# Kernel optimization log

Measured on AMD Instinct MI355X. Metric: run time of the kernel, lower is better.

The kernel has to match this reference:

```python
import jax, jax.numpy as jnp
import numpy as np

K = 4096       # num_codebook_vectors
D = 256        # latent_dim
BETA = 0.25


def setup_inputs() -> dict:
    key = jax.random.key(0)
    k1, k2 = jax.random.split(key)
    z = jax.random.normal(k1, (16, D, 64, 64), dtype=jnp.float32)
    # nn.Embedding init: uniform(-1/K, 1/K)
    emb = jax.random.uniform(k2, (K, D), dtype=jnp.float32, minval=-1.0 / K, maxval=1.0 / K)
    return {"z": z, "emb": emb}


def reference(z, emb):
    B, C, H, W = z.shape
    zp = jnp.transpose(z, (0, 2, 3, 1))            # [B,H,W,C]
    zf = zp.reshape(-1, C)                          # [N,C]
    # squared L2 distances: ||z||^2 + ||e||^2 - 2 z.e
    d = (jnp.sum(zf * zf, axis=1, keepdims=True)
         + jnp.sum(emb * emb, axis=1)
         - 2.0 * jnp.matmul(zf, emb.T))             # [N,K]
    idx = jnp.argmin(d, axis=1)                     # [N]
    z_q = jnp.take(emb, idx, axis=0).reshape(zp.shape)  # [B,H,W,C]
    loss = (jnp.mean((jax.lax.stop_gradient(z_q) - zp) ** 2)
            + BETA * jnp.mean((z_q - jax.lax.stop_gradient(zp)) ** 2))
    # straight-through estimator
    z_q = zp + jax.lax.stop_gradient(z_q - zp)
    z_q = jnp.transpose(z_q, (0, 3, 1, 2))          # back to NCHW
    return z_q, idx, loss
```

## Files before the change

kernel.cpp:

```cpp
#include <hip/hip_runtime.h>
#include <math.h>

#define KCODES 4096
#define DIM    256
#define HW     4096
#define NPIX   65536
#define NQ     16777216
#define EPSW   3.0e-4f

typedef _Float16 f16x8 __attribute__((ext_vector_type(8)));
typedef float    f32x4 __attribute__((ext_vector_type(4)));

#define SWZ(x) ((x) ^ ((((x) >> 6) & 7) << 4))

static __device__ __forceinline__ void gld16(const void* g, void* l) {
    __builtin_amdgcn_global_load_lds(
        (const __attribute__((address_space(1))) void*)g,
        (__attribute__((address_space(3))) void*)l, 16, 0, 0);
}

#define INS4(V, I, dd, kk) do { \
  if ((dd) < V[3]) { \
    if ((dd) < V[1]) { \
      V[3]=V[2]; I[3]=I[2]; V[2]=V[1]; I[2]=I[1]; \
      if ((dd) < V[0]) { V[1]=V[0]; I[1]=I[0]; V[0]=(dd); I[0]=(kk); } \
      else             { V[1]=(dd); I[1]=(kk); } \
    } else { \
      if ((dd) < V[2]) { V[3]=V[2]; I[3]=I[2]; V[2]=(dd); I[2]=(kk); } \
      else             { V[3]=(dd); I[3]=(kk); } \
    } } } while(0)

#define INS8(V, I, dd, kk) do { \
  if ((dd) < V[7]) { \
    if ((dd) < V[3]) { \
      V[7]=V[6];I[7]=I[6];V[6]=V[5];I[6]=I[5];V[5]=V[4];I[5]=I[4];V[4]=V[3];I[4]=I[3]; \
      if ((dd) < V[1]) { \
        V[3]=V[2];I[3]=I[2];V[2]=V[1];I[2]=I[1]; \
        if ((dd) < V[0]) { V[1]=V[0];I[1]=I[0];V[0]=(dd);I[0]=(kk); } \
        else             { V[1]=(dd);I[1]=(kk); } \
      } else { \
        if ((dd) < V[2]) { V[3]=V[2];I[3]=I[2];V[2]=(dd);I[2]=(kk); } \
        else             { V[3]=(dd);I[3]=(kk); } \
      } \
    } else { \
      if ((dd) < V[5]) { \
        V[7]=V[6];I[7]=I[6];V[6]=V[5];I[6]=I[5]; \
        if ((dd) < V[4]) { V[5]=V[4];I[5]=I[4];V[4]=(dd);I[4]=(kk); } \
        else             { V[5]=(dd);I[5]=(kk); } \
      } else { \
        if ((dd) < V[6]) { V[7]=V[6];I[7]=I[6];V[6]=(dd);I[6]=(kk); } \
        else             { V[7]=(dd);I[7]=(kk); } \
      } \
    } } } while(0)

__global__ __launch_bounds__(256) void ee_np_kernel(const float* __restrict__ emb,
                                                    float* __restrict__ ee) {
#pragma clang fp contract(off)
    const int k = blockIdx.x * 256 + threadIdx.x;
    const float* a = emb + (size_t)k * DIM;
    float res[2];
    #pragma unroll
    for (int h = 0; h < 2; ++h) {
        const float* b = a + h * 128;
        float r[8];
        #pragma unroll
        for (int j = 0; j < 8; ++j) { const float x = b[j]; r[j] = x * x; }
        for (int i = 8; i < 128; i += 8) {
            #pragma unroll
            for (int j = 0; j < 8; ++j) { const float x = b[i + j]; r[j] += x * x; }
        }
        res[h] = ((r[0] + r[1]) + (r[2] + r[3])) + ((r[4] + r[5]) + (r[6] + r[7]));
    }
    ee[k] = res[0] + res[1];
}

__global__ __launch_bounds__(256) void zz_np_kernel(const float* __restrict__ z,
                                                    float* __restrict__ zz) {
#pragma clang fp contract(off)
    const int n  = blockIdx.x * 256 + threadIdx.x;
    const int b  = n >> 12;
    const int hw = n & (HW - 1);
    const float* base = z + (size_t)b * DIM * HW + hw;
    float res[2];
    #pragma unroll
    for (int h = 0; h < 2; ++h) {
        const float* p = base + (size_t)(h * 128) * HW;
        float r[8];
        #pragma unroll
        for (int j = 0; j < 8; ++j) { const float x = p[(size_t)j * HW]; r[j] = x * x; }
        for (int i = 8; i < 128; i += 8) {
            #pragma unroll
            for (int j = 0; j < 8; ++j) { const float x = p[(size_t)(i + j) * HW]; r[j] += x * x; }
        }
        res[h] = ((r[0] + r[1]) + (r[2] + r[3])) + ((r[4] + r[5]) + (r[6] + r[7]));
    }
    zz[n] = res[0] + res[1];
}

__device__ float np_dist(const float* __restrict__ z, const float* __restrict__ emb,
                         const float* __restrict__ zz, const float* __restrict__ ee,
                         int n, int k) {
    const int b = n >> 12, hw = n & (HW - 1);
    const float* zp = z + (size_t)b * DIM * HW + hw;
    const float* ep = emb + (size_t)k * DIM;
    float m = 0.0f;
    for (int i = 0; i < DIM; ++i) m = fmaf(zp[(size_t)i * HW], ep[i], m);
    const float t = zz[n] + ee[k];
    return t - 2.0f * m;
}

__global__ __launch_bounds__(256) void cvt_emb_kernel(const float* __restrict__ emb,
                                                      ushort* __restrict__ eh) {
    const int t = threadIdx.x;
    const int k = blockIdx.x * 4 + (t >> 6);
    const int seg = t & 63;
    const float4 v = *reinterpret_cast<const float4*>(emb + (size_t)k * DIM + seg * 4);
    union H4 { _Float16 h[4]; short4 s; } uh;
    const float vv[4] = {v.x, v.y, v.z, v.w};
    #pragma unroll
    for (int j = 0; j < 4; ++j) uh.h[j] = (_Float16)(vv[j] * 4096.0f);
    const int s = seg >> 3;
    const int y  = (k & 127) * 64 + (seg & 7) * 8;
    const int ys = y ^ ((k & 7) << 4);
    const size_t addr = (size_t)(k >> 7) * 32768 + s * 4096 + (ys >> 1);
    *reinterpret_cast<short4*>(eh + addr) = uh.s;
}

__global__ __launch_bounds__(256) void cvt_z_kernel(const float* __restrict__ z,
                                                    ushort* __restrict__ zh) {
    __shared__ float ls[64][65];
    const int t = threadIdx.x;
    const int bid = blockIdx.x;
    const int b = bid >> 8, cc = (bid >> 6) & 3, hh = bid & 63;
    const int col = t & 63, r0 = t >> 6;
    #pragma unroll
    for (int i = 0; i < 16; ++i) {
        const int r = i * 4 + r0;
        ls[r][col] = z[((size_t)(b * DIM + cc * 64 + r)) * HW + hh * 64 + col];
    }
    __syncthreads();
    const int pxl = t >> 2, cseg = t & 3;
    const int px = b * HW + hh * 64 + pxl;
    const int sg = cc * 2 + (cseg >> 1);
    union H8 { _Float16 h[8]; int4 v; } ha, hb;
    #pragma unroll
    for (int j = 0; j < 16; ++j) {
        const float val = ls[cseg * 16 + j][pxl];
        if (j < 8) ha.h[j] = (_Float16)val;
        else       hb.h[j - 8] = (_Float16)val;
    }
    const size_t chunk = (size_t)(px >> 7) * 32768 + sg * 4096;
    const int y1  = (px & 127) * 64 + (cseg & 1) * 32;
    const int msk = (px & 7) << 4;
    *reinterpret_cast<int4*>(zh + chunk + ((y1 ^ msk) >> 1))        = ha.v;
    *reinterpret_cast<int4*>(zh + chunk + (((y1 + 16) ^ msk) >> 1)) = hb.v;
}

__global__ __launch_bounds__(256, 2) void gemm_kernel(const ushort* __restrict__ eh,
                                                      const ushort* __restrict__ zh,
                                                      const float* __restrict__ ee,
                                                      const float* __restrict__ zz,
                                                      float* __restrict__ top8v,
                                                      int* __restrict__ top8i,
                                                      float* __restrict__ m3f) {
    __shared__ __align__(16) char zt[65536];
    __shared__ __align__(16) char et[2][8192];

    const int t = threadIdx.x;
    const int lane = t & 63, w = t >> 6, wr = w >> 1, wc = w & 1;
    const int l15 = lane & 15, l4 = lane >> 4;
    const int px0 = blockIdx.x * 128;
    const int lo = t * 16;
    const int wb = w * 1024;

    {
        const char* zg = (const char*)zh + (size_t)blockIdx.x * 65536;
        #pragma unroll
        for (int i = 0; i < 16; ++i)
            gld16(zg + i * 4096 + lo, zt + i * 4096 + wb);
        const char* eg = (const char*)eh;
        gld16(eg + lo,        et[0] + wb);
        gld16(eg + 4096 + lo, et[0] + 4096 + wb);
    }
    float zzr[4];
    #pragma unroll
    for (int ni = 0; ni < 4; ++ni) zzr[ni] = zz[px0 + wc * 64 + ni * 16 + l15];
    __syncthreads();

    float Tv[4][4]; int Ti[4][4];
    #pragma unroll
    for (int ni = 0; ni < 4; ++ni)
        #pragma unroll
        for (int j = 0; j < 4; ++j) { Tv[ni][j] = 3.0e38f; Ti[ni][j] = 0; }

    f32x4 acc[4][4];
    float eer[4][4];
    int cur = 0;

    for (int t7 = 0; t7 < 256; ++t7) {
        const int p = t7 >> 3, s = t7 & 7;
        if (t7 < 255) {
            const char* eg = (const char*)eh + (size_t)(t7 + 1) * 8192;
            gld16(eg + lo,        et[cur ^ 1] + wb);
            gld16(eg + 4096 + lo, et[cur ^ 1] + 4096 + wb);
        }
        if (s == 0) {
            #pragma unroll
            for (int mi = 0; mi < 4; ++mi) {
                #pragma unroll
                for (int r = 0; r < 4; ++r)
                    eer[mi][r] = ee[p * 128 + wr * 64 + mi * 16 + l4 * 4 + r];
                #pragma unroll
                for (int ni = 0; ni < 4; ++ni)
                    acc[mi][ni] = (f32x4){0.0f, 0.0f, 0.0f, 0.0f};
            }
        }
        f16x8 bH[4];
        #pragma unroll
        for (int ni = 0; ni < 4; ++ni) {
            const int ob = s * 8192 + SWZ((wc * 64 + ni * 16 + l15) * 64 + l4 * 16);
            bH[ni] = *reinterpret_cast<const f16x8*>(zt + ob);
        }
        #pragma unroll
        for (int mi = 0; mi < 4; ++mi) {
            const int oa = SWZ((wr * 64 + mi * 16 + l15) * 64 + l4 * 16);
            const f16x8 aH = *reinterpret_cast<const f16x8*>(et[cur] + oa);
            #pragma unroll
            for (int ni = 0; ni < 4; ++ni)
                acc[mi][ni] = __builtin_amdgcn_mfma_f32_16x16x32_f16(aH, bH[ni], acc[mi][ni], 0, 0, 0);
        }
        if (s == 7) {
            #pragma unroll
            for (int ni = 0; ni < 4; ++ni) {
                const float zzc = zzr[ni];
                #pragma unroll
                for (int mi = 0; mi < 4; ++mi) {
                    #pragma unroll
                    for (int r = 0; r < 4; ++r) {
                        const float tt = zzc + eer[mi][r];
                        const float d = fmaf(acc[mi][ni][r], -4.8828125e-4f, tt);
                        const int k = p * 128 + wr * 64 + mi * 16 + l4 * 4 + r;
                        INS4(Tv[ni], Ti[ni], d, k);
                    }
                }
            }
        }
        __syncthreads();
        cur ^= 1;
    }

    float (*mv)[128][8]  = reinterpret_cast<float (*)[128][8]>(&zt[0]);
    int   (*mi_)[128][8] = reinterpret_cast<int (*)[128][8]>(&zt[16384]);
    float (*m3s)[128]    = reinterpret_cast<float (*)[128]>(&zt[32768]);

    #pragma unroll
    for (int ni = 0; ni < 4; ++ni) {
        float fv[8]; int fi[8];
        #pragma unroll
        for (int j = 0; j < 4; ++j) { fv[j] = Tv[ni][j]; fi[j] = Ti[ni][j]; }
        #pragma unroll
        for (int j = 4; j < 8; ++j) { fv[j] = 3.0e38f; fi[j] = 0; }
        float m3 = Tv[ni][3];
        #pragma unroll
        for (int m = 16; m <= 32; m <<= 1) {
            float ov[8]; int oi[8];
            #pragma unroll
            for (int j = 0; j < 8; ++j) {
                ov[j] = __shfl_xor(fv[j], m, 64);
                oi[j] = __shfl_xor(fi[j], m, 64);
            }
            const float om = __shfl_xor(m3, m, 64);
            #pragma unroll
            for (int j = 0; j < 8; ++j) INS8(fv, fi, ov[j], oi[j]);
            m3 = fminf(m3, om);
        }
        if (lane < 16) {
            const int c = wc * 64 + ni * 16 + lane;
            #pragma unroll
            for (int j = 0; j < 8; ++j) { mv[wr][c][j] = fv[j]; mi_[wr][c][j] = fi[j]; }
            m3s[wr][c] = m3;
        }
    }
    __syncthreads();
    if (t < 128) {
        float fv[8]; int fi[8];
        #pragma unroll
        for (int j = 0; j < 8; ++j) { fv[j] = mv[0][t][j]; fi[j] = mi_[0][t][j]; }
        #pragma unroll
        for (int j = 0; j < 8; ++j) INS8(fv, fi, mv[1][t][j], mi_[1][t][j]);
        const float m3 = fminf(m3s[0][t], m3s[1][t]);
        const int px = px0 + t;
        *reinterpret_cast<float4*>(top8v + (size_t)px * 8)     = make_float4(fv[0], fv[1], fv[2], fv[3]);
        *reinterpret_cast<float4*>(top8v + (size_t)px * 8 + 4) = make_float4(fv[4], fv[5], fv[6], fv[7]);
        *reinterpret_cast<int4*>(top8i + (size_t)px * 8)       = make_int4(fi[0], fi[1], fi[2], fi[3]);
        *reinterpret_cast<int4*>(top8i + (size_t)px * 8 + 4)   = make_int4(fi[4], fi[5], fi[6], fi[7]);
        m3f[px] = m3;
    }
}

__global__ __launch_bounds__(256) void resolve_kernel(const float* __restrict__ z,
                                                      const float* __restrict__ emb,
                                                      const float* __restrict__ zz,
                                                      const float* __restrict__ ee,
                                                      const float* __restrict__ top8v,
                                                      const int* __restrict__ top8i,
                                                      const float* __restrict__ m3f,
                                                      int* __restrict__ idxf,
                                                      int* __restrict__ cnt,
                                                      int* __restrict__ rlist) {
    const int n = blockIdx.x * 256 + threadIdx.x;
    float v[8]; int id[8];
    {
        const float4 v0 = *reinterpret_cast<const float4*>(top8v + (size_t)n * 8);
        const float4 v1 = *reinterpret_cast<const float4*>(top8v + (size_t)n * 8 + 4);
        const int4   i0 = *reinterpret_cast<const int4*>(top8i + (size_t)n * 8);
        const int4   i1 = *reinterpret_cast<const int4*>(top8i + (size_t)n * 8 + 4);
        v[0]=v0.x; v[1]=v0.y; v[2]=v0.z; v[3]=v0.w; v[4]=v1.x; v[5]=v1.y; v[6]=v1.z; v[7]=v1.w;
        id[0]=i0.x; id[1]=i0.y; id[2]=i0.z; id[3]=i0.w; id[4]=i1.x; id[5]=i1.y; id[6]=i1.z; id[7]=i1.w;
    }
    const float lim = v[0] + EPSW;
    if (v[7] <= lim || m3f[n] <= lim) {
        idxf[n] = id[0];
        const int pos = atomicAdd(cnt, 1);
        rlist[pos] = n;
        return;
    }
    if (v[1] > lim) { idxf[n] = id[0]; return; }
    int ck[8]; int nc = 0;
    for (int j = 0; j < 8; ++j) if (v[j] <= lim) ck[nc++] = id[j];
    for (int a = 0; a < nc - 1; ++a)
        for (int b2 = a + 1; b2 < nc; ++b2)
            if (ck[b2] < ck[a]) { int tmp = ck[a]; ck[a] = ck[b2]; ck[b2] = tmp; }
    float best = 0.0f; int bk = -1;
    for (int a = 0; a < nc; ++a) {
        const float d = np_dist(z, emb, zz, ee, n, ck[a]);
        if (bk < 0 || d < best) { best = d; bk = ck[a]; }
    }
    idxf[n] = bk;
}

__global__ __launch_bounds__(256) void rescan_kernel(const float* __restrict__ z,
                                                     const float* __restrict__ emb,
                                                     const float* __restrict__ zz,
                                                     const float* __restrict__ ee,
                                                     const int* __restrict__ cnt,
                                                     const int* __restrict__ rlist,
                                                     int* __restrict__ idxf) {
#pragma clang fp contract(off)
    __shared__ float ls[DIM];
    __shared__ float wv[4];
    __shared__ int   wk[4];
    const int t = threadIdx.x;
    const int lane = t & 63, w = t >> 6;
    const int count = *cnt;
    for (int e = blockIdx.x; e < count; e += gridDim.x) {
        const int n = rlist[e];
        const int b = n >> 12, hw = n & (HW - 1);
        __syncthreads();
        ls[t] = z[((size_t)(b * DIM + t)) * HW + hw];
        __syncthreads();
        const float zzn = zz[n];
        float bestd = 3.0e38f; int besti = 0x7fffffff;
        for (int j = 0; j < 16; ++j) {
            const int k = t + j * 256;
            const float* ep = emb + (size_t)k * DIM;
            float m = 0.0f;
            for (int i = 0; i < DIM; ++i) m = fmaf(ls[i], ep[i], m);
            const float d = (zzn + ee[k]) - 2.0f * m;
            if (d < bestd || (d == bestd && k < besti)) { bestd = d; besti = k; }
        }
        #pragma unroll
        for (int off = 32; off >= 1; off >>= 1) {
            const float od = __shfl_down(bestd, off, 64);
            const int   ok = __shfl_down(besti, off, 64);
            if (od < bestd || (od == bestd && ok < besti)) { bestd = od; besti = ok; }
        }
        if (lane == 0) { wv[w] = bestd; wk[w] = besti; }
        __syncthreads();
        if (t == 0) {
            float bd = wv[0]; int bi = wk[0];
            #pragma unroll
            for (int q = 1; q < 4; ++q)
                if (wv[q] < bd || (wv[q] == bd && wk[q] < bi)) { bd = wv[q]; bi = wk[q]; }
            idxf[n] = bi;
        }
    }
}

__global__ __launch_bounds__(256) void gather_kernel(const float* __restrict__ z,
                                                     const float* __restrict__ emb,
                                                     const int* __restrict__ idxf,
                                                     float* __restrict__ out,
                                                     float* __restrict__ part) {
    __shared__ int   idx_s[32];
    __shared__ float wred[4];
    const int tid = threadIdx.x;
    const int tx = tid & 31, ty = tid >> 5;
    const int m0 = blockIdx.x * 32;
    const int bimg = m0 >> 12, hw0 = m0 & (HW - 1);
    if (tid < 32) {
        const int ii = idxf[m0 + tid];
        idx_s[tid] = ii;
        out[NQ + m0 + tid] = (float)ii;
    }
    __syncthreads();
    float lsum = 0.0f;
    const size_t ebase = (size_t)idx_s[tx] * DIM;
    for (int it = 0; it < DIM / 8; ++it) {
        const int c = it * 8 + ty;
        const float e = emb[ebase + c];
        const size_t zoff = ((size_t)(bimg * DIM + c)) * HW + hw0 + tx;
        out[zoff] = e;
        const float diff = e - z[zoff];
        lsum += diff * diff;
    }
    #pragma unroll
    for (int off = 32; off >= 1; off >>= 1) lsum += __shfl_down(lsum, off, 64);
    if ((tid & 63) == 0) wred[tid >> 6] = lsum;
    __syncthreads();
    if (tid == 0) part[blockIdx.x] = wred[0] + wred[1] + wred[2] + wred[3];
}

__global__ __launch_bounds__(256) void loss_kernel(const float* __restrict__ part,
                                                   int nblk, float* __restrict__ out) {
    __shared__ float wred[4];
    const int tid = threadIdx.x;
    float s = 0.0f;
    for (int i = tid; i < nblk; i += 256) s += part[i];
    #pragma unroll
    for (int off = 32; off >= 1; off >>= 1) s += __shfl_down(s, off, 64);
    if ((tid & 63) == 0) wred[tid >> 6] = s;
    __syncthreads();
    if (tid == 0) {
        const float total = wred[0] + wred[1] + wred[2] + wred[3];
        out[NQ + NPIX] = 1.25f * total / 16777216.0f;
    }
}

#define MP 32
#define KC 128
#define DC 32
__global__ __launch_bounds__(256) void safe_dist_kernel(const float* __restrict__ z,
                                                        const float* __restrict__ emb,
                                                        const float* __restrict__ ee,
                                                        const float* __restrict__ zz,
                                                        float* __restrict__ out,
                                                        float* __restrict__ part) {
    __shared__ float zs[MP][DIM + 4];
    __shared__ float est[DC][KC + 4];
    __shared__ float ee_s[KC];
    __shared__ float zz_s[MP];
    __shared__ float red_v[MP][33];
    __shared__ int   red_i[MP][33];
    __shared__ int   idx_s[MP];
    __shared__ float wred[4];

    const int tid = threadIdx.x;
    const int tx = tid & 31, ty = tid >> 5;
    const int m0 = blockIdx.x * MP;
    const int bimg = m0 >> 12, hw0 = m0 & (HW - 1);

    for (int c = ty; c < DIM; c += 8)
        zs[tx][c] = z[((size_t)(bimg * DIM + c)) * HW + hw0 + tx];
    if (tid < MP) zz_s[tid] = zz[m0 + tid];

    float minv[4]; int mini[4];
    #pragma unroll
    for (int p = 0; p < 4; ++p) { minv[p] = 3.0e38f; mini[p] = 0; }
    const int rl = tid >> 3, cl = tid & 7;

    for (int kc = 0; kc < KCODES / KC; ++kc) {
        float acc[4][4];
        #pragma unroll
        for (int p = 0; p < 4; ++p)
            #pragma unroll
            for (int q = 0; q < 4; ++q) acc[p][q] = 0.0f;
        for (int dc = 0; dc < DIM / DC; ++dc) {
            __syncthreads();
            if (dc == 0 && tid < KC) ee_s[tid] = ee[kc * KC + tid];
            #pragma unroll
            for (int it = 0; it < 4; ++it) {
                const int kl = it * 32 + rl;
                const float4 v = *reinterpret_cast<const float4*>(
                    emb + (size_t)(kc * KC + kl) * DIM + dc * DC + cl * 4);
                est[cl * 4 + 0][kl] = v.x;
                est[cl * 4 + 1][kl] = v.y;
                est[cl * 4 + 2][kl] = v.z;
                est[cl * 4 + 3][kl] = v.w;
            }
            __syncthreads();
            #pragma unroll
            for (int g = 0; g < DC / 4; ++g) {
                float4 zr[4];
                #pragma unroll
                for (int p = 0; p < 4; ++p)
                    zr[p] = *reinterpret_cast<const float4*>(&zs[ty * 4 + p][dc * DC + g * 4]);
                float4 er[4];
                #pragma unroll
                for (int j = 0; j < 4; ++j)
                    er[j] = *reinterpret_cast<const float4*>(&est[g * 4 + j][tx * 4]);
                #pragma unroll
                for (int p = 0; p < 4; ++p) {
                    acc[p][0] = fmaf(zr[p].x, er[0].x, acc[p][0]);
                    acc[p][0] = fmaf(zr[p].y, er[1].x, acc[p][0]);
                    acc[p][0] = fmaf(zr[p].z, er[2].x, acc[p][0]);
                    acc[p][0] = fmaf(zr[p].w, er[3].x, acc[p][0]);
                    acc[p][1] = fmaf(zr[p].x, er[0].y, acc[p][1]);
                    acc[p][1] = fmaf(zr[p].y, er[1].y, acc[p][1]);
                    acc[p][1] = fmaf(zr[p].z, er[2].y, acc[p][1]);
                    acc[p][1] = fmaf(zr[p].w, er[3].y, acc[p][1]);
                    acc[p][2] = fmaf(zr[p].x, er[0].z, acc[p][2]);
                    acc[p][2] = fmaf(zr[p].y, er[1].z, acc[p][2]);
                    acc[p][2] = fmaf(zr[p].z, er[2].z, acc[p][2]);
                    acc[p][2] = fmaf(zr[p].w, er[3].z, acc[p][2]);
                    acc[p][3] = fmaf(zr[p].x, er[0].w, acc[p][3]);
                    acc[p][3] = fmaf(zr[p].y, er[1].w, acc[p][3]);
                    acc[p][3] = fmaf(zr[p].z, er[2].w, acc[p][3]);
                    acc[p][3] = fmaf(zr[p].w, er[3].w, acc[p][3]);
                }
            }
        }
        #pragma unroll
        for (int q = 0; q < 4; ++q) {
            const int kg = kc * KC + tx * 4 + q;
            const float en = ee_s[tx * 4 + q];
            #pragma unroll
            for (int p = 0; p < 4; ++p) {
                const float t = zz_s[ty * 4 + p] + en;
                const float d = t - 2.0f * acc[p][q];
                if (d < minv[p]) { minv[p] = d; mini[p] = kg; }
            }
        }
    }
    #pragma unroll
    for (int p = 0; p < 4; ++p) {
        red_v[ty * 4 + p][tx] = minv[p];
        red_i[ty * 4 + p][tx] = mini[p];
    }
    __syncthreads();
    if (tid < MP) {
        float bvv = red_v[tid][0]; int bii = red_i[tid][0];
        for (int q = 1; q < 32; ++q) {
            const float vq = red_v[tid][q]; const int iq = red_i[tid][q];
            if (vq < bvv || (vq == bvv && iq < bii)) { bvv = vq; bii = iq; }
        }
        idx_s[tid] = bii;
        out[NQ + m0 + tid] = (float)bii;
    }
    __syncthreads();
    float lsum = 0.0f;
    const size_t ebase = (size_t)idx_s[tx] * DIM;
    for (int it = 0; it < DIM / 8; ++it) {
        const int c = it * 8 + ty;
        const float e = emb[ebase + c];
        out[((size_t)(bimg * DIM + c)) * HW + hw0 + tx] = e;
        const float diff = e - zs[tx][c];
        lsum += diff * diff;
    }
    #pragma unroll
    for (int off = 32; off >= 1; off >>= 1) lsum += __shfl_down(lsum, off, 64);
    if ((tid & 63) == 0) wred[tid >> 6] = lsum;
    __syncthreads();
    if (tid == 0) part[blockIdx.x] = wred[0] + wred[1] + wred[2] + wred[3];
}

extern "C" void kernel_launch(void* const* d_in, const int* in_sizes, int n_in,
                              void* d_out, int out_size, void* d_ws, size_t ws_size,
                              hipStream_t stream) {
    const float* z   = (const float*)d_in[0];
    const float* emb = (const float*)d_in[1];
    float* out = (float*)d_out;
    char*  ws  = (char*)d_ws;

    float* zz   = (float*)(ws + 0);
    float* ee   = (float*)(ws + 262144);
    float* part = (float*)(ws + 278528);
    int*   cnt  = (int*)  (ws + 286720);
    int*   rlst = (int*)  (ws + 290816);
    int*   idxf = (int*)  (ws + 552960);
    float* t8v  = (float*)(ws + 1048576);
    int*   t8i  = (int*)  (ws + 3145728);
    ushort* eh  = (ushort*)(ws + 5242880);
    ushort* zh  = (ushort*)(ws + 7340032);
    float* m3f  = (float*)(ws + 40894464);
    const size_t REQ = 74448896;

    ee_np_kernel<<<KCODES / 256, 256, 0, stream>>>(emb, ee);
    zz_np_kernel<<<NPIX / 256, 256, 0, stream>>>(z, zz);

    if (ws_size >= REQ) {
        hipMemsetAsync(cnt, 0, 4, stream);
        cvt_emb_kernel<<<KCODES / 4, 256, 0, stream>>>(emb, eh);
        cvt_z_kernel<<<4096, 256, 0, stream>>>(z, zh);
        gemm_kernel<<<NPIX / 128, 256, 0, stream>>>(eh, zh, ee, zz, t8v, t8i, m3f);
        resolve_kernel<<<NPIX / 256, 256, 0, stream>>>(z, emb, zz, ee, t8v, t8i, m3f, idxf, cnt, rlst);
        rescan_kernel<<<2048, 256, 0, stream>>>(z, emb, zz, ee, cnt, rlst, idxf);
        gather_kernel<<<NPIX / 32, 256, 0, stream>>>(z, emb, idxf, out, part);
        loss_kernel<<<1, 256, 0, stream>>>(part, NPIX / 32, out);
    } else {
        safe_dist_kernel<<<NPIX / MP, 256, 0, stream>>>(z, emb, ee, zz, out, part);
        loss_kernel<<<1, 256, 0, stream>>>(part, NPIX / MP, out);
    }
}
```

Baseline: 571.2 us.

## Load codebook A-fragments directly from global memory, drop LDS double-buffer and barriers

Removes the double-buffered LDS staging of codebook tiles and the per-step __syncthreads. Each wave now reads its f16 codebook fragments straight from global memory (relying on L1/L2 caching), with the loop restructured into an outer loop over 128-code panels and an unrolled inner loop over 8 K-slices. Precomputed swizzled offsets are hoisted out of the loop. This trades barrier overhead and LDS traffic for global-memory latency on the A operand, which is no longer prefetched ahead of use.

```diff
diff --git a/kernel.cpp b/kernel.cpp
--- a/kernel.cpp
+++ b/kernel.cpp
@@ -164,7 +164,6 @@
                                                       int* __restrict__ top8i,
                                                       float* __restrict__ m3f) {
     __shared__ __align__(16) char zt[65536];
-    __shared__ __align__(16) char et[2][8192];
 
     const int t = threadIdx.x;
     const int lane = t & 63, w = t >> 6, wr = w >> 1, wc = w & 1;
@@ -178,13 +177,20 @@
         #pragma unroll
         for (int i = 0; i < 16; ++i)
             gld16(zg + i * 4096 + lo, zt + i * 4096 + wb);
-        const char* eg = (const char*)eh;
-        gld16(eg + lo,        et[0] + wb);
-        gld16(eg + 4096 + lo, et[0] + 4096 + wb);
     }
     float zzr[4];
     #pragma unroll
     for (int ni = 0; ni < 4; ++ni) zzr[ni] = zz[px0 + wc * 64 + ni * 16 + l15];
+
+    int aoff[4];
+    #pragma unroll
+    for (int mi = 0; mi < 4; ++mi)
+        aoff[mi] = SWZ((wr * 64 + mi * 16 + l15) * 64 + l4 * 16) >> 1;
+    int boff[4];
+    #pragma unroll
+    for (int ni = 0; ni < 4; ++ni)
+        boff[ni] = SWZ((wc * 64 + ni * 16 + l15) * 64 + l4 * 16);
+
     __syncthreads();
 
     float Tv[4][4]; int Ti[4][4];
@@ -193,62 +199,55 @@
         #pragma unroll
         for (int j = 0; j < 4; ++j) { Tv[ni][j] = 3.0e38f; Ti[ni][j] = 0; }
 
-    f32x4 acc[4][4];
-    float eer[4][4];
-    int cur = 0;
-
-    for (int t7 = 0; t7 < 256; ++t7) {
-        const int p = t7 >> 3, s = t7 & 7;
-        if (t7 < 255) {
-            const char* eg = (const char*)eh + (size_t)(t7 + 1) * 8192;
-            gld16(eg + lo,        et[cur ^ 1] + wb);
-            gld16(eg + 4096 + lo, et[cur ^ 1] + 4096 + wb);
-        }
-        if (s == 0) {
+    for (int p = 0; p < 32; ++p) {
+        float eer[4][4];
+        #pragma unroll
+        for (int mi = 0; mi < 4; ++mi)
+            #pragma unroll
+            for (int r = 0; r < 4; ++r)
+                eer[mi][r] = ee[p * 128 + wr * 64 + mi * 16 + l4 * 4 + r];
+
+        f32x4 acc[4][4];
+        #pragma unroll
+        for (int mi = 0; mi < 4; ++mi)
+            #pragma unroll
+            for (int ni = 0; ni < 4; ++ni)
+                acc[mi][ni] = (f32x4){0.0f, 0.0f, 0.0f, 0.0f};
+
+        #pragma unroll
+        for (int s = 0; s < 8; ++s) {
+            const ushort* eb = eh + (size_t)p * 32768 + s * 4096;
+            f16x8 aH[4];
+            #pragma unroll
+            for (int mi = 0; mi < 4; ++mi)
+                aH[mi] = *reinterpret_cast<const f16x8*>(eb + aoff[mi]);
+            f16x8 bH[4];
+            #pragma unroll
+            for (int ni = 0; ni < 4; ++ni)
+                bH[ni] = *reinterpret_cast<const f16x8*>(zt + s * 8192 + boff[ni]);
+            #pragma unroll
+            for (int mi = 0; mi < 4; ++mi)
+                #pragma unroll
+                for (int ni = 0; ni < 4; ++ni)
+                    acc[mi][ni] = __builtin_amdgcn_mfma_f32_16x16x32_f16(aH[mi], bH[ni], acc[mi][ni], 0, 0, 0);
+        }
+        #pragma unroll
+        for (int ni = 0; ni < 4; ++ni) {
+            const float zzc = zzr[ni];
             #pragma unroll
             for (int mi = 0; mi < 4; ++mi) {
                 #pragma unroll
-                for (int r = 0; r < 4; ++r)
-                    eer[mi][r] = ee[p * 128 + wr * 64 + mi * 16 + l4 * 4 + r];
-                #pragma unroll
-                for (int ni = 0; ni < 4; ++ni)
-                    acc[mi][ni] = (f32x4){0.0f, 0.0f, 0.0f, 0.0f};
-            }
-        }
-        f16x8 bH[4];
-        #pragma unroll
-        for (int ni = 0; ni < 4; ++ni) {
-            const int ob = s * 8192 + SWZ((wc * 64 + ni * 16 + l15) * 64 + l4 * 16);
-            bH[ni] = *reinterpret_cast<const f16x8*>(zt + ob);
-        }
-        #pragma unroll
-        for (int mi = 0; mi < 4; ++mi) {
-            const int oa = SWZ((wr * 64 + mi * 16 + l15) * 64 + l4 * 16);
-            const f16x8 aH = *reinterpret_cast<const f16x8*>(et[cur] + oa);
-            #pragma unroll
-            for (int ni = 0; ni < 4; ++ni)
-                acc[mi][ni] = __builtin_amdgcn_mfma_f32_16x16x32_f16(aH, bH[ni], acc[mi][ni], 0, 0, 0);
-        }
-        if (s == 7) {
-            #pragma unroll
-            for (int ni = 0; ni < 4; ++ni) {
-                const float zzc = zzr[ni];
-                #pragma unroll
-                for (int mi = 0; mi < 4; ++mi) {
-                    #pragma unroll
-                    for (int r = 0; r < 4; ++r) {
-                        const float tt = zzc + eer[mi][r];
-                        const float d = fmaf(acc[mi][ni][r], -4.8828125e-4f, tt);
-                        const int k = p * 128 + wr * 64 + mi * 16 + l4 * 4 + r;
-                        INS4(Tv[ni], Ti[ni], d, k);
-                    }
+                for (int r = 0; r < 4; ++r) {
+                    const float tt = zzc + eer[mi][r];
+                    const float d = fmaf(acc[mi][ni][r], -4.8828125e-4f, tt);
+                    const int k = p * 128 + wr * 64 + mi * 16 + l4 * 4 + r;
+                    INS4(Tv[ni], Ti[ni], d, k);
                 }
             }
         }
-        __syncthreads();
-        cur ^= 1;
-    }
-
+    }
+
+    __syncthreads();
     float (*mv)[128][8]  = reinterpret_cast<float (*)[128][8]>(&zt[0]);
     int   (*mi_)[128][8] = reinterpret_cast<int (*)[128][8]>(&zt[16384]);
     float (*m3s)[128]    = reinterpret_cast<float (*)[128]>(&zt[32768]);
```

Result: slower. 728.4 us (+27.5%).
